# Optimization experiments

Measured on AMD Instinct MI355X. Metric: run time of the kernel, lower is better.

## Reference

```python
import jax, jax.numpy as jnp
import numpy as np

N_NODES = 100000
N_EDGES = 1600000
IN_CH = 128


def _init_linear(key, fan_in, fan_out, bias=True):
    kw, kb = jax.random.split(key)
    bound = 1.0 / np.sqrt(fan_in)
    W = jax.random.uniform(kw, (fan_in, fan_out), jnp.float32, -bound, bound)
    if bias:
        b = jax.random.uniform(kb, (fan_out,), jnp.float32, -bound, bound)
        return W, b
    return W, None


def setup_inputs() -> dict:
    key = jax.random.key(0)
    ks = jax.random.split(key, 10)
    x = jax.random.normal(ks[0], (N_NODES, IN_CH), jnp.float32)
    edge_index = jax.random.randint(ks[1], (2, N_EDGES), 0, N_NODES, dtype=jnp.int64)
    # PyG SAGEConv: out = lin_l(mean_agg) + lin_r(x); lin_l has bias, lin_r does not.
    w1l, b1l = _init_linear(ks[2], IN_CH, 128)
    w1r, _ = _init_linear(ks[3], IN_CH, 128, bias=False)
    w2l, b2l = _init_linear(ks[4], 128, 64)
    w2r, _ = _init_linear(ks[5], 128, 64, bias=False)
    w3l, b3l = _init_linear(ks[6], 64, 32)
    w3r, _ = _init_linear(ks[7], 64, 32, bias=False)
    wc, bc = _init_linear(ks[8], 32, 2)
    return {
        "x": x, "edge_index": edge_index,
        "w1l": w1l, "b1l": b1l, "w1r": w1r,
        "w2l": w2l, "b2l": b2l, "w2r": w2r,
        "w3l": w3l, "b3l": b3l, "w3r": w3r,
        "wc": wc, "bc": bc,
    }


def _sage_conv(h, edge_index, wl, bl, wr):
    # mean aggregation of source-node features onto destination nodes
    src, dst = edge_index[0], edge_index[1]
    n = h.shape[0]
    agg = jax.ops.segment_sum(h[src], dst, num_segments=n)            # [N, d]
    deg = jax.ops.segment_sum(jnp.ones((src.shape[0],), h.dtype), dst, num_segments=n)
    mean = agg / jnp.maximum(deg, 1.0)[:, None]
    return mean @ wl + bl + h @ wr


def reference(x, edge_index, w1l, b1l, w1r, w2l, b2l, w2r, w3l, b3l, w3r, wc, bc):
    # dropout(p=0.3) is identity in eval mode
    h = jax.nn.relu(_sage_conv(x, edge_index, w1l, b1l, w1r))
    h = jax.nn.relu(_sage_conv(h, edge_index, w2l, b2l, w2r))
    h = jax.nn.relu(_sage_conv(h, edge_index, w3l, b3l, w3r))
    return h @ wc + bc  # [N, 2] logits
```

## Files before the change

kernel.cpp:

```cpp
#include <hip/hip_runtime.h>


#define EBLK 4096

__global__ __launch_bounds__(256) void bucket_hist_kernel(
    const int* __restrict__ ei, int* __restrict__ cnt, int E)
{
    __shared__ int h[256];
    int tid = threadIdx.x;
    h[tid] = 0;
    __syncthreads();
    int e0 = blockIdx.x * EBLK;
    int ecnt = min(EBLK, E - e0);
    for (int i = tid; i < ecnt; i += 256)
        atomicAdd(&h[ei[E + e0 + i] >> 9], 1);
    __syncthreads();
    if (h[tid]) atomicAdd(&cnt[tid], h[tid]);
}

__global__ __launch_bounds__(256) void bucket_scan_kernel(
    const int* __restrict__ cnt, int* __restrict__ bbase,
    int* __restrict__ bcur, int nb, int E)
{
    __shared__ int s[256];
    int t = threadIdx.x;
    s[t] = (t < nb) ? cnt[t] : 0;
    __syncthreads();
    for (int off = 1; off < 256; off <<= 1) {
        int v = 0;
        if (t >= off) v = s[t - off];
        __syncthreads();
        if (t >= off) s[t] += v;
        __syncthreads();
    }
    int ex = (t == 0) ? 0 : s[t - 1];
    if (t < nb) { bbase[t] = ex; bcur[t] = ex; }
    if (t == 0) bbase[nb] = E;
}

__global__ __launch_bounds__(256) void bin_scatter_kernel(
    const int* __restrict__ ei, int* __restrict__ bcur,
    uint2* __restrict__ ebuf, int E)
{
    __shared__ int h[256];
    __shared__ int start[256];
    int tid = threadIdx.x;
    int e0 = blockIdx.x * EBLK;
    int ecnt = min(EBLK, E - e0);
    h[tid] = 0;
    start[tid] = 0;
    __syncthreads();
    for (int i = tid; i < ecnt; i += 256)
        atomicAdd(&h[ei[E + e0 + i] >> 9], 1);
    __syncthreads();
    if (h[tid] > 0) start[tid] = atomicAdd(&bcur[tid], h[tid]);
    __syncthreads();
    h[tid] = start[tid];
    __syncthreads();
    for (int i = tid; i < ecnt; i += 256) {
        int src = ei[e0 + i];
        int dst = ei[E + e0 + i];
        int pos = atomicAdd(&h[dst >> 9], 1);
        ebuf[pos] = make_uint2((unsigned)src, (unsigned)dst);
    }
}

__global__ __launch_bounds__(512) void bucket_fill_kernel(
    const uint2* __restrict__ ebuf, const int* __restrict__ bbase,
    int* __restrict__ offs, float* __restrict__ invd,
    int* __restrict__ csr, int N, int E)
{
    __shared__ int deg[512];
    __shared__ int s[512];
    int b = blockIdx.x;
    int lo = b << 9;
    int base = bbase[b];
    int end = bbase[b + 1];
    int tid = threadIdx.x;
    deg[tid] = 0;
    __syncthreads();
    for (int i = base + tid; i < end; i += 512)
        atomicAdd(&deg[(int)ebuf[i].y - lo], 1);
    __syncthreads();
    int d = deg[tid];
    s[tid] = d;
    __syncthreads();
    for (int off = 1; off < 512; off <<= 1) {
        int v = 0;
        if (tid >= off) v = s[tid - off];
        __syncthreads();
        if (tid >= off) s[tid] += v;
        __syncthreads();
    }
    int ex = s[tid] - d;
    int n = lo + tid;
    if (n < N) {
        offs[n] = base + ex;
        invd[n] = 1.0f / (float)(d > 0 ? d : 1);
    }
    __syncthreads();
    deg[tid] = ex;
    __syncthreads();
    for (int i = base + tid; i < end; i += 512) {
        uint2 ed = ebuf[i];
        int pos = atomicAdd(&deg[(int)ed.y - lo], 1);
        csr[base + pos] = (int)ed.x;
    }
    if (b == 0 && tid == 0) offs[N] = E;
}


__device__ inline unsigned short f2bf(float f) {
    unsigned int u = __float_as_uint(f);
    return (unsigned short)((u + 0x7fffu + ((u >> 16) & 1u)) >> 16);
}

__device__ inline float bflo(unsigned int u) { return __uint_as_float(u << 16); }
__device__ inline float bfhi(unsigned int u) { return __uint_as_float(u & 0xffff0000u); }

__global__ void f32_to_bf16_kernel(const float* __restrict__ in,
                                   unsigned short* __restrict__ out, int n4) {
    int i = blockIdx.x * blockDim.x + threadIdx.x;
    if (i < n4) {
        float4 v = *(const float4*)(in + (size_t)i * 4);
        ushort4 o;
        o.x = f2bf(v.x); o.y = f2bf(v.y); o.z = f2bf(v.z); o.w = f2bf(v.w);
        *(ushort4*)(out + (size_t)i * 4) = o;
    }
}


__device__ inline void addbf8(float* a, uint4 v) {
    a[0] += bflo(v.x); a[1] += bfhi(v.x);
    a[2] += bflo(v.y); a[3] += bfhi(v.y);
    a[4] += bflo(v.z); a[5] += bfhi(v.z);
    a[6] += bflo(v.w); a[7] += bfhi(v.w);
}

template <int D>
__global__ __launch_bounds__(256) void aggregate_bf16_kernel(
    const unsigned short* __restrict__ hb, const int* __restrict__ offs,
    const int* __restrict__ csr, const float* __restrict__ invd,
    unsigned short* __restrict__ meanb, int nN)
{
    constexpr int LPR = D / 8;
    constexpr int G = 64 / LPR;
    int wid = blockIdx.x * 4 + (threadIdx.x >> 6);
    int lane = threadIdx.x & 63;
    if (wid >= nN) return;
    int o0 = offs[wid], o1 = offs[wid + 1];
    const int p = lane / LPR;
    const int col = (lane % LPR) * 8;

    float a0[8] = {0.f, 0.f, 0.f, 0.f, 0.f, 0.f, 0.f, 0.f};
    float a1[8] = {0.f, 0.f, 0.f, 0.f, 0.f, 0.f, 0.f, 0.f};
    int j = o0;
    for (; j + 2 * G <= o1; j += 2 * G) {
        int s0 = csr[j + p];
        int s1 = csr[j + G + p];
        uint4 v0 = *(const uint4*)(hb + (size_t)s0 * D + col);
        uint4 v1 = *(const uint4*)(hb + (size_t)s1 * D + col);
        addbf8(a0, v0);
        addbf8(a1, v1);
    }
    if (j + G <= o1) {
        int s0 = csr[j + p];
        uint4 v0 = *(const uint4*)(hb + (size_t)s0 * D + col);
        addbf8(a0, v0);
        j += G;
    }
    if (j < o1 && p < o1 - j) {
        int s1 = csr[j + p];
        uint4 v1 = *(const uint4*)(hb + (size_t)s1 * D + col);
        addbf8(a1, v1);
    }
#pragma unroll
    for (int q = 0; q < 8; q++) a0[q] += a1[q];

#pragma unroll
    for (int m = LPR; m < 64; m <<= 1) {
#pragma unroll
        for (int q = 0; q < 8; q++) a0[q] += __shfl_xor(a0[q], m);
    }

    if (lane < LPR) {
        float iv = invd[wid];
        uint4 o;
        o.x = (unsigned)f2bf(a0[0] * iv) | ((unsigned)f2bf(a0[1] * iv) << 16);
        o.y = (unsigned)f2bf(a0[2] * iv) | ((unsigned)f2bf(a0[3] * iv) << 16);
        o.z = (unsigned)f2bf(a0[4] * iv) | ((unsigned)f2bf(a0[5] * iv) << 16);
        o.w = (unsigned)f2bf(a0[6] * iv) | ((unsigned)f2bf(a0[7] * iv) << 16);
        *(uint4*)(meanb + (size_t)wid * D + col) = o;
    }
}


typedef short short8 __attribute__((ext_vector_type(8)));
typedef short short4v __attribute__((ext_vector_type(4)));
typedef float f32x4 __attribute__((ext_vector_type(4)));

__global__ void swizzle_w_kernel(const float* __restrict__ W,
                                 unsigned short* __restrict__ Ws,
                                 int K, int M) {
    int t = blockIdx.x * blockDim.x + threadIdx.x;
    int KB = K >> 5;
    int total = (M >> 4) * KB * 64;
    if (t >= total) return;
    int l = t & 63;
    int kbc = t >> 6;
    int kb = kbc % KB;
    int c = kbc / KB;
    int km = kb * 32 + ((l >> 4) << 2);
    int m = (c << 4) + (l & 15);
    unsigned short o[8];
#pragma unroll
    for (int j = 0; j < 8; j++) {
        int k = km + (j >> 2) * 16 + (j & 3);
        o[j] = f2bf(W[(size_t)k * M + m]);
    }
    *(uint4*)(Ws + (size_t)t * 8) = *(uint4*)o;
}

template <int K, int M>
__global__ __launch_bounds__(512) void gemm_mfma(
    const unsigned short* __restrict__ A1, const unsigned short* __restrict__ A2,
    const unsigned short* __restrict__ w1s, const unsigned short* __restrict__ w2s,
    const float* __restrict__ bias, float* __restrict__ out,
    unsigned short* __restrict__ outb, int nN)
{
    constexpr int KB = K / 32;
    constexpr int CB = M / 16;
    const int l = threadIdx.x & 63;
    const int wv = threadIdx.x >> 6;
    const int rowbase = blockIdx.x * 128 + wv * 16;
    if (rowbase >= nN) return;
    const int arow = rowbase + (l & 15);
    const int ksub = (l >> 4) << 2;

    f32x4 acc[CB];
#pragma unroll
    for (int c = 0; c < CB; c++) acc[c] = (f32x4){0.f, 0.f, 0.f, 0.f};

    const unsigned short* a1p = A1 + (size_t)arow * K + ksub;
    const unsigned short* a2p = A2 + (size_t)arow * K + ksub;

#pragma unroll
    for (int kb = 0; kb < KB; kb++) {
        short4v l1 = *(const short4v*)(a1p + kb * 32);
        short4v h1 = *(const short4v*)(a1p + kb * 32 + 16);
        short4v l2 = *(const short4v*)(a2p + kb * 32);
        short4v h2 = *(const short4v*)(a2p + kb * 32 + 16);
        short8 a1 = {l1[0], l1[1], l1[2], l1[3], h1[0], h1[1], h1[2], h1[3]};
        short8 a2 = {l2[0], l2[1], l2[2], l2[3], h2[0], h2[1], h2[2], h2[3]};
#pragma unroll
        for (int c = 0; c < CB; c++) {
            short8 b1 = *(const short8*)(w1s + ((size_t)(c * KB + kb) * 64 + l) * 8);
            acc[c] = __builtin_amdgcn_mfma_f32_16x16x32_bf16(a1, b1, acc[c], 0, 0, 0);
            short8 b2 = *(const short8*)(w2s + ((size_t)(c * KB + kb) * 64 + l) * 8);
            acc[c] = __builtin_amdgcn_mfma_f32_16x16x32_bf16(a2, b2, acc[c], 0, 0, 0);
        }
    }

    const int orow = rowbase + ((l >> 4) << 2);
#pragma unroll
    for (int c = 0; c < CB; c++) {
        int col = (c << 4) + (l & 15);
        float bv = bias[col];
#pragma unroll
        for (int r = 0; r < 4; r++) {
            float v = fmaxf(acc[c][r] + bv, 0.f);
            size_t idx = (size_t)(orow + r) * M + col;
            if (out) out[idx] = v;
            if (outb) outb[idx] = f2bf(v);
        }
    }
}


__global__ void classifier_kernel(const float* __restrict__ h,
                                  const float* __restrict__ wc,
                                  const float* __restrict__ bc,
                                  float* __restrict__ out, int nN) {
    int n = blockIdx.x * blockDim.x + threadIdx.x;
    if (n >= nN) return;
    float a0 = bc[0], a1 = bc[1];
    const float* row = h + (size_t)n * 32;
#pragma unroll
    for (int k = 0; k < 32; k++) {
        float v = row[k];
        a0 = fmaf(v, wc[k * 2 + 0], a0);
        a1 = fmaf(v, wc[k * 2 + 1], a1);
    }
    out[n * 2 + 0] = a0;
    out[n * 2 + 1] = a1;
}


extern "C" void kernel_launch(void* const* d_in, const int* in_sizes, int n_in,
                              void* d_out, int out_size, void* d_ws, size_t ws_size,
                              hipStream_t stream) {
    const float* x   = (const float*)d_in[0];
    const int*   ei  = (const int*)d_in[1];
    const float* w1l = (const float*)d_in[2];
    const float* b1l = (const float*)d_in[3];
    const float* w1r = (const float*)d_in[4];
    const float* w2l = (const float*)d_in[5];
    const float* b2l = (const float*)d_in[6];
    const float* w2r = (const float*)d_in[7];
    const float* w3l = (const float*)d_in[8];
    const float* b3l = (const float*)d_in[9];
    const float* w3r = (const float*)d_in[10];
    const float* wc  = (const float*)d_in[11];
    const float* bc  = (const float*)d_in[12];
    float* out = (float*)d_out;

    const int N = in_sizes[0] / 128;
    const int E = in_sizes[1] / 2;
    const int NBq = (N + 511) >> 9;

    char* p = (char*)d_ws;
    auto alloc = [&](size_t bytes) {
        char* r = p;
        p += (bytes + 511) & ~(size_t)511;
        return r;
    };
    int*   offs   = (int*)  alloc(((size_t)N + 1) * 4);
    float* invd   = (float*)alloc((size_t)N * 4);
    int*   bcnt   = (int*)  alloc(256 * 4);
    int*   bbase  = (int*)  alloc(257 * 4);
    int*   bcur   = (int*)  alloc(256 * 4);
    uint2* ebuf   = (uint2*)alloc((size_t)E * 8);
    int*   csr    = (int*)  alloc((size_t)E * 4);
    float* h3     = (float*)alloc((size_t)N * 32 * 4);
    unsigned short* xb    = (unsigned short*)alloc((size_t)N * 128 * 2);
    unsigned short* h1b   = (unsigned short*)alloc((size_t)N * 128 * 2);
    unsigned short* h2b   = (unsigned short*)alloc((size_t)N * 64 * 2);
    unsigned short* meanb = (unsigned short*)alloc((size_t)N * 128 * 2);
    unsigned short* w1ls  = (unsigned short*)alloc(128 * 128 * 2);
    unsigned short* w1rs  = (unsigned short*)alloc(128 * 128 * 2);
    unsigned short* w2ls  = (unsigned short*)alloc(128 * 64 * 2);
    unsigned short* w2rs  = (unsigned short*)alloc(128 * 64 * 2);
    unsigned short* w3ls  = (unsigned short*)alloc(64 * 32 * 2);
    unsigned short* w3rs  = (unsigned short*)alloc(64 * 32 * 2);

    hipMemsetAsync(bcnt, 0, 256 * 4, stream);

    int eb4 = (E + EBLK - 1) / EBLK;
    bucket_hist_kernel<<<eb4, 256, 0, stream>>>(ei, bcnt, E);
    bucket_scan_kernel<<<1, 256, 0, stream>>>(bcnt, bbase, bcur, NBq, E);
    bin_scatter_kernel<<<eb4, 256, 0, stream>>>(ei, bcur, ebuf, E);
    bucket_fill_kernel<<<NBq, 512, 0, stream>>>(ebuf, bbase, offs, invd, csr, N, E);

    int n4 = N * 128 / 4;
    f32_to_bf16_kernel<<<(n4 + 255) / 256, 256, 0, stream>>>(x, xb, n4);

    swizzle_w_kernel<<<(128 * 128 / 8 + 255) / 256, 256, 0, stream>>>(w1l, w1ls, 128, 128);
    swizzle_w_kernel<<<(128 * 128 / 8 + 255) / 256, 256, 0, stream>>>(w1r, w1rs, 128, 128);
    swizzle_w_kernel<<<(128 * 64 / 8 + 255) / 256, 256, 0, stream>>>(w2l, w2ls, 128, 64);
    swizzle_w_kernel<<<(128 * 64 / 8 + 255) / 256, 256, 0, stream>>>(w2r, w2rs, 128, 64);
    swizzle_w_kernel<<<(64 * 32 / 8 + 255) / 256, 256, 0, stream>>>(w3l, w3ls, 64, 32);
    swizzle_w_kernel<<<(64 * 32 / 8 + 255) / 256, 256, 0, stream>>>(w3r, w3rs, 64, 32);

    int ab = (N + 3) / 4;
    int gm = (N + 127) / 128;

    aggregate_bf16_kernel<128><<<ab, 256, 0, stream>>>(xb, offs, csr, invd, meanb, N);
    gemm_mfma<128, 128><<<gm, 512, 0, stream>>>(meanb, xb, w1ls, w1rs, b1l, nullptr, h1b, N);

    aggregate_bf16_kernel<128><<<ab, 256, 0, stream>>>(h1b, offs, csr, invd, meanb, N);
    gemm_mfma<128, 64><<<gm, 512, 0, stream>>>(meanb, h1b, w2ls, w2rs, b2l, nullptr, h2b, N);

    aggregate_bf16_kernel<64><<<ab, 256, 0, stream>>>(h2b, offs, csr, invd, meanb, N);
    gemm_mfma<64, 32><<<gm, 512, 0, stream>>>(meanb, h2b, w3ls, w3rs, b3l, h3, nullptr, N);

    classifier_kernel<<<(N + 255) / 256, 256, 0, stream>>>(h3, wc, bc, out, N);
}
```

Measured before the change: 325.6 us.

## Transform-then-aggregate for layers 2 and 3 to gather narrower features

For layers 2 and 3, the node features are first multiplied by both weight matrices (the split GEMM), and the neighbour mean is then gathered over the projected, narrower features. This relies on mean aggregation commuting with the linear map. The bias, the self term and the ReLU move into the aggregation epilogue. The aim is to cut gather traffic, since layer 2 now gathers 64-wide rows instead of 128-wide and layer 3 gathers 32-wide instead of 64-wide. In exchange there are extra intermediate writes and reads, and the projected values are rounded to bf16 before they are summed.

Result: faster. 299.1 us (median of 2 runs) (-8.1%).

```diff
diff --git a/kernel.cpp b/kernel.cpp
--- a/kernel.cpp
+++ b/kernel.cpp
@@ -191,6 +191,81 @@
         o.z = (unsigned)f2bf(a0[4] * iv) | ((unsigned)f2bf(a0[5] * iv) << 16);
         o.w = (unsigned)f2bf(a0[6] * iv) | ((unsigned)f2bf(a0[7] * iv) << 16);
         *(uint4*)(meanb + (size_t)wid * D + col) = o;
+    }
+}
+
+
+template <int D, bool F32OUT>
+__global__ __launch_bounds__(256) void agg_finish_kernel(
+    const unsigned short* __restrict__ pb, const unsigned short* __restrict__ qb,
+    const float* __restrict__ bias, const int* __restrict__ offs,
+    const int* __restrict__ csr, const float* __restrict__ invd,
+    unsigned short* __restrict__ outb, float* __restrict__ outf, int nN)
+{
+    constexpr int LPR = D / 8;
+    constexpr int G = 64 / LPR;
+    int wid = blockIdx.x * 4 + (threadIdx.x >> 6);
+    int lane = threadIdx.x & 63;
+    if (wid >= nN) return;
+    int o0 = offs[wid], o1 = offs[wid + 1];
+    const int p = lane / LPR;
+    const int col = (lane % LPR) * 8;
+
+    float a0[8] = {0.f, 0.f, 0.f, 0.f, 0.f, 0.f, 0.f, 0.f};
+    float a1[8] = {0.f, 0.f, 0.f, 0.f, 0.f, 0.f, 0.f, 0.f};
+    int j = o0;
+    for (; j + 2 * G <= o1; j += 2 * G) {
+        int s0 = csr[j + p];
+        int s1 = csr[j + G + p];
+        uint4 v0 = *(const uint4*)(pb + (size_t)s0 * D + col);
+        uint4 v1 = *(const uint4*)(pb + (size_t)s1 * D + col);
+        addbf8(a0, v0);
+        addbf8(a1, v1);
+    }
+    if (j + G <= o1) {
+        int s0 = csr[j + p];
+        uint4 v0 = *(const uint4*)(pb + (size_t)s0 * D + col);
+        addbf8(a0, v0);
+        j += G;
+    }
+    if (j < o1 && p < o1 - j) {
+        int s1 = csr[j + p];
+        uint4 v1 = *(const uint4*)(pb + (size_t)s1 * D + col);
+        addbf8(a1, v1);
+    }
+#pragma unroll
+    for (int q = 0; q < 8; q++) a0[q] += a1[q];
+
+#pragma unroll
+    for (int m = LPR; m < 64; m <<= 1) {
+#pragma unroll
+        for (int q = 0; q < 8; q++) a0[q] += __shfl_xor(a0[q], m);
+    }
+
+    if (lane < LPR) {
+        float iv = invd[wid];
+        uint4 qv = *(const uint4*)(qb + (size_t)wid * D + col);
+        float qf[8];
+        qf[0] = bflo(qv.x); qf[1] = bfhi(qv.x);
+        qf[2] = bflo(qv.y); qf[3] = bfhi(qv.y);
+        qf[4] = bflo(qv.z); qf[5] = bfhi(qv.z);
+        qf[6] = bflo(qv.w); qf[7] = bfhi(qv.w);
+        float r[8];
+#pragma unroll
+        for (int q = 0; q < 8; q++)
+            r[q] = fmaxf(a0[q] * iv + qf[q] + bias[col + q], 0.f);
+        if (F32OUT) {
+            float* dst = outf + (size_t)wid * D + col;
+            *(float4*)(dst)     = make_float4(r[0], r[1], r[2], r[3]);
+            *(float4*)(dst + 4) = make_float4(r[4], r[5], r[6], r[7]);
+        } else {
+            uint4 o;
+            o.x = (unsigned)f2bf(r[0]) | ((unsigned)f2bf(r[1]) << 16);
+            o.y = (unsigned)f2bf(r[2]) | ((unsigned)f2bf(r[3]) << 16);
+            o.z = (unsigned)f2bf(r[4]) | ((unsigned)f2bf(r[5]) << 16);
+            o.w = (unsigned)f2bf(r[6]) | ((unsigned)f2bf(r[7]) << 16);
+            *(uint4*)(outb + (size_t)wid * D + col) = o;
+        }
     }
 }
 
@@ -272,6 +347,57 @@
             size_t idx = (size_t)(orow + r) * M + col;
             if (out) out[idx] = v;
             if (outb) outb[idx] = f2bf(v);
+        }
+    }
+}
+
+template <int K, int M>
+__global__ __launch_bounds__(512) void gemm_mfma_split(
+    const unsigned short* __restrict__ A,
+    const unsigned short* __restrict__ w1s, const unsigned short* __restrict__ w2s,
+    unsigned short* __restrict__ pb, unsigned short* __restrict__ qb, int nN)
+{
+    constexpr int KB = K / 32;
+    constexpr int CB = M / 16;
+    const int l = threadIdx.x & 63;
+    const int wv = threadIdx.x >> 6;
+    const int rowbase = blockIdx.x * 128 + wv * 16;
+    if (rowbase >= nN) return;
+    const int arow = rowbase + (l & 15);
+    const int ksub = (l >> 4) << 2;
+
+    f32x4 accp[CB], accq[CB];
+#pragma unroll
+    for (int c = 0; c < CB; c++) {
+        accp[c] = (f32x4){0.f, 0.f, 0.f, 0.f};
+        accq[c] = (f32x4){0.f, 0.f, 0.f, 0.f};
+    }
+
+    const unsigned short* ap = A + (size_t)arow * K + ksub;
+
+#pragma unroll
+    for (int kb = 0; kb < KB; kb++) {
+        short4v lo = *(const short4v*)(ap + kb * 32);
+        short4v hi = *(const short4v*)(ap + kb * 32 + 16);
+        short8 a = {lo[0], lo[1], lo[2], lo[3], hi[0], hi[1], hi[2], hi[3]};
+#pragma unroll
+        for (int c = 0; c < CB; c++) {
+            short8 b1 = *(const short8*)(w1s + ((size_t)(c * KB + kb) * 64 + l) * 8);
+            accp[c] = __builtin_amdgcn_mfma_f32_16x16x32_bf16(a, b1, accp[c], 0, 0, 0);
+            short8 b2 = *(const short8*)(w2s + ((size_t)(c * KB + kb) * 64 + l) * 8);
+            accq[c] = __builtin_amdgcn_mfma_f32_16x16x32_bf16(a, b2, accq[c], 0, 0, 0);
+        }
+    }
+
+    const int orow = rowbase + ((l >> 4) << 2);
+#pragma unroll
+    for (int c = 0; c < CB; c++) {
+        int col = (c << 4) + (l & 15);
+#pragma unroll
+        for (int r = 0; r < 4; r++) {
+            size_t idx = (size_t)(orow + r) * M + col;
+            pb[idx] = f2bf(accp[c][r]);
+            qb[idx] = f2bf(accq[c][r]);
         }
     }
 }
@@ -336,6 +462,10 @@
     unsigned short* h1b   = (unsigned short*)alloc((size_t)N * 128 * 2);
     unsigned short* h2b   = (unsigned short*)alloc((size_t)N * 64 * 2);
     unsigned short* meanb = (unsigned short*)alloc((size_t)N * 128 * 2);
+    unsigned short* p2b   = (unsigned short*)alloc((size_t)N * 64 * 2);
+    unsigned short* q2b   = (unsigned short*)alloc((size_t)N * 64 * 2);
+    unsigned short* p3b   = (unsigned short*)alloc((size_t)N * 32 * 2);
+    unsigned short* q3b   = (unsigned short*)alloc((size_t)N * 32 * 2);
     unsigned short* w1ls  = (unsigned short*)alloc(128 * 128 * 2);
     unsigned short* w1rs  = (unsigned short*)alloc(128 * 128 * 2);
     unsigned short* w2ls  = (unsigned short*)alloc(128 * 64 * 2);
@@ -367,11 +497,11 @@
     aggregate_bf16_kernel<128><<<ab, 256, 0, stream>>>(xb, offs, csr, invd, meanb, N);
     gemm_mfma<128, 128><<<gm, 512, 0, stream>>>(meanb, xb, w1ls, w1rs, b1l, nullptr, h1b, N);
 
-    aggregate_bf16_kernel<128><<<ab, 256, 0, stream>>>(h1b, offs, csr, invd, meanb, N);
-    gemm_mfma<128, 64><<<gm, 512, 0, stream>>>(meanb, h1b, w2ls, w2rs, b2l, nullptr, h2b, N);
-
-    aggregate_bf16_kernel<64><<<ab, 256, 0, stream>>>(h2b, offs, csr, invd, meanb, N);
-    gemm_mfma<64, 32><<<gm, 512, 0, stream>>>(meanb, h2b, w3ls, w3rs, b3l, h3, nullptr, N);
+    gemm_mfma_split<128, 64><<<gm, 512, 0, stream>>>(h1b, w2ls, w2rs, p2b, q2b, N);
+    agg_finish_kernel<64, false><<<ab, 256, 0, stream>>>(p2b, q2b, b2l, offs, csr, invd, h2b, nullptr, N);
+
+    gemm_mfma_split<64, 32><<<gm, 512, 0, stream>>>(h2b, w3ls, w3rs, p3b, q3b, N);
+    agg_finish_kernel<32, true><<<ab, 256, 0, stream>>>(p3b, q3b, b3l, offs, csr, invd, nullptr, h3, N);
 
     classifier_kernel<<<(N + 255) / 256, 256, 0, stream>>>(h3, wc, bc, out, N);
 }
```
